# Optimization experiments

Hardware: AMD Instinct MI355X
Metric: run time of the kernel (lower is better)

The kernel has to match this reference:

```python
import jax, jax.numpy as jnp
import numpy as np

BN, SN = 16, 64
C, T, FY, FX = 480, 8, 28, 28
OS = 8            # roialign output_size
NDF = 256
K = 64            # n_clusters
ALPHA = 1.0
IMG_W, IMG_H = 1920.0, 1080.0
SPATIAL_SCALE = 1.0


def _roi_align(feat, boxes):
    """torchvision RoIAlign with sampling_ratio=1, aligned=True.
    feat: [bn, C, H, W]; boxes: [bn, sn, 4] (x1,y1,x2,y2) in feature coords.
    Returns [bn, sn, C, OS, OS]."""
    bn, c, H, W = feat.shape
    xy1 = boxes[..., 0:2] * SPATIAL_SCALE - 0.5   # aligned=True offset
    xy2 = boxes[..., 2:4] * SPATIAL_SCALE - 0.5
    bin_wh = (xy2 - xy1) / OS                     # [bn,sn,2]
    ctr = jnp.arange(OS, dtype=feat.dtype) + 0.5  # one sample per bin (ratio=1)
    xs = xy1[..., 0:1] + ctr * bin_wh[..., 0:1]   # [bn,sn,OS]
    ys = xy1[..., 1:2] + ctr * bin_wh[..., 1:2]
    X = xs[:, :, None, :]                         # [bn,sn,1,OS]
    Y = ys[:, :, :, None]                         # [bn,sn,OS,1]
    valid = (Y > -1.0) & (Y < H) & (X > -1.0) & (X < W)
    x = jnp.clip(X, 0.0, W - 1.0)
    y = jnp.clip(Y, 0.0, H - 1.0)
    x0 = jnp.floor(x).astype(jnp.int32)
    y0 = jnp.floor(y).astype(jnp.int32)
    x1 = jnp.minimum(x0 + 1, W - 1)
    y1 = jnp.minimum(y0 + 1, H - 1)
    lx = x - x0
    ly = y - y0
    fhw = jnp.transpose(feat, (0, 2, 3, 1))       # [bn,H,W,C]
    g = jax.vmap(lambda f, yy, xx: f[yy, xx])     # broadcasting gather -> [bn,sn,OS,OS,C]
    v00 = g(fhw, y0, x0); v01 = g(fhw, y0, x1)
    v10 = g(fhw, y1, x0); v11 = g(fhw, y1, x1)
    wy0, wy1 = (1.0 - ly)[..., None], ly[..., None]
    wx0, wx1 = (1.0 - lx)[..., None], lx[..., None]
    out = v00 * wy0 * wx0 + v01 * wy0 * wx1 + v10 * wy1 * wx0 + v11 * wy1 * wx1
    out = jnp.where(valid[..., None], out, 0.0)
    return jnp.transpose(out, (0, 1, 4, 2, 3))    # [bn,sn,C,OS,OS] (torch layout)


def setup_inputs() -> dict:
    key = jax.random.key(0)
    ks = jax.random.split(key, 6)
    z_vis = jax.random.normal(ks[0], (BN, C, T, FY, FX), jnp.float32)
    # valid boxes (x1<x2, y1<y2), fully inside the image -> no NaN padding rows
    tl = jax.random.uniform(ks[1], (BN, SN, 2)) * jnp.array([IMG_W * 0.5, IMG_H * 0.5])
    wh = jax.random.uniform(ks[2], (BN, SN, 2)) * jnp.array([IMG_W * 0.4, IMG_H * 0.4]) + 16.0
    bboxs = jnp.concatenate([tl, tl + wh], axis=-1).astype(jnp.float32)
    W_vis = jax.random.normal(ks[3], (C * OS * OS, NDF), jnp.float32) / np.sqrt(C * OS * OS)
    b_vis = jnp.zeros((NDF,), jnp.float32)
    W_spc = jax.random.normal(ks[4], (1, NDF), jnp.float32)
    b_spc = jnp.zeros((NDF,), jnp.float32)
    centroids = jax.random.normal(ks[5], (K, NDF), jnp.float32) * 0.1
    return {"z_vis": z_vis, "bboxs": bboxs, "W_vis": W_vis, "b_vis": b_vis,
            "W_spc": W_spc, "b_spc": b_spc, "centroids": centroids}


def reference(z_vis, bboxs, W_vis, b_vis, W_spc, b_spc, centroids):
    bn, sn = bboxs.shape[:2]
    # scale image-coord boxes to feature-map coords
    scale = jnp.array([FX / IMG_W, FY / IMG_H], dtype=z_vis.dtype)
    boxes_f = (bboxs.reshape(bn, sn, 2, 2) * scale).reshape(bn, sn, 4)
    feat = z_vis[:, :, -1]                                   # last temporal frame [bn,C,fy,fx]
    roi = _roi_align(feat, boxes_f).reshape(bn, sn, -1)      # [bn,sn,C*OS*OS]
    z_v = roi @ W_vis + b_vis                                # visual embedding [bn,sn,NDF]
    # spatial embedding: normalized distance of bbox center to image center (detached)
    b2 = bboxs.reshape(bn, sn, 2, 2)
    ctr = b2[:, :, 0] + (b2[:, :, 1] - b2[:, :, 0]) * 0.5    # [bn,sn,2]
    img_c = jnp.array([IMG_W / 2.0, IMG_H / 2.0], dtype=z_vis.dtype)
    norms = jnp.linalg.norm(ctr - img_c, axis=-1, keepdims=True) / jnp.linalg.norm(img_c)
    norms = jax.lax.stop_gradient(norms)                     # .detach() in original
    z_s = norms @ W_spc + b_spc                              # [bn,sn,NDF]
    z = z_v + z_s
    # Student-t soft assignment on L2 distance (NOT squared, as in the source)
    d = jnp.linalg.norm(z[:, :, None, :] - centroids, axis=-1)   # [bn,sn,K]
    s_un = (1.0 + d / ALPHA) ** (-(ALPHA + 1.0) / 2.0)
    s = s_un / jnp.sum(s_un, axis=-1, keepdims=True)
    c = jnp.argmax(s, axis=-1)
    return z, s, c
```

## Files before the change

### kernel.cpp

```cpp
#include <hip/hip_runtime.h>
#include <cstdint>
#include <cstddef>

#define BN_   16
#define C_    480
#define T_    8
#define FY_   28
#define FX_   28
#define NDF_  256
#define KC_   64
#define M_    1024
#define KD_   30720
#define PLANE_ 784
#define CHSTRIDE_ (T_*PLANE_)
#define CT_   (C_*CHSTRIDE_)
#define KS_   32
#define KCH_  960
#define BK_   32
#define NSTEP_ (KCH_/BK_)
#define MT_   32
#define APAD_ 40

typedef __attribute__((ext_vector_type(8))) short bf16x8;
typedef __attribute__((ext_vector_type(4))) float f32x4;

__device__ __forceinline__ unsigned rne_bf16(float f) {
    union { float f; unsigned u; } v; v.f = f;
    return v.u + 0x7FFFu + ((v.u >> 16) & 1u);
}
__device__ __forceinline__ float bfbits_to_f(unsigned r) {
    union { unsigned u; float f; } v; v.u = r & 0xFFFF0000u;
    return v.f;
}

__global__ __launch_bounds__(256)
void convert_w(const float* __restrict__ W, unsigned short* __restrict__ Wt_hi,
               unsigned short* __restrict__ Wt_lo) {
    __shared__ unsigned short th[64][68];
    __shared__ unsigned short tl[64][68];
    const int k0 = blockIdx.x * 64, n0 = blockIdx.y * 64;
    const int t = threadIdx.x;
    const int sub = t >> 4, off4 = (t & 15) * 4;
    #pragma unroll
    for (int p = 0; p < 4; ++p) {
        const int kr = p * 16 + sub;
        const float4 v = *(const float4*)&W[(size_t)(k0 + kr) * NDF_ + n0 + off4];
        const float vv[4] = { v.x, v.y, v.z, v.w };
        #pragma unroll
        for (int e = 0; e < 4; ++e) {
            const unsigned rh = rne_bf16(vv[e]);
            const unsigned rl = rne_bf16(vv[e] - bfbits_to_f(rh));
            th[kr][off4 + e] = (unsigned short)(rh >> 16);
            tl[kr][off4 + e] = (unsigned short)(rl >> 16);
        }
    }
    __syncthreads();
    #pragma unroll
    for (int p = 0; p < 4; ++p) {
        const int nr = p * 16 + sub;
        ushort4 oh, ol;
        oh.x = th[off4 + 0][nr]; oh.y = th[off4 + 1][nr];
        oh.z = th[off4 + 2][nr]; oh.w = th[off4 + 3][nr];
        ol.x = tl[off4 + 0][nr]; ol.y = tl[off4 + 1][nr];
        ol.z = tl[off4 + 2][nr]; ol.w = tl[off4 + 3][nr];
        *(ushort4*)&Wt_hi[(size_t)(n0 + nr) * KD_ + k0 + off4] = oh;
        *(ushort4*)&Wt_lo[(size_t)(n0 + nr) * KD_ + k0 + off4] = ol;
    }
}

__global__ void convert_cent(const float* __restrict__ cent, float* __restrict__ centT) {
    const int k = blockIdx.x;
    const int j = threadIdx.x;
    centT[(size_t)j * KC_ + k] = cent[(size_t)k * NDF_ + j];
}

__global__ __launch_bounds__(256, 4)
void gemm_fused(const float* __restrict__ z_vis, const unsigned short* __restrict__ Wt_hi,
                const unsigned short* __restrict__ Wt_lo, const float* __restrict__ bboxs,
                float* __restrict__ part) {
    __shared__ short Ah[MT_ * APAD_];
    __shared__ short Al[MT_ * APAD_];
    __shared__ unsigned short Bh[256 * 32];
    __shared__ unsigned short Bl[256 * 32];
    const int t = threadIdx.x;
    const int ks = blockIdx.x, mi = blockIdx.y;
    const int lane = t & 63, wid = t >> 6;
    const int kbase = ks * KCH_;

    const int m = t >> 3, q = t & 7;
    const int roi = mi * MT_ + m;
    const int bn = mi >> 1;

    int xi0[4], xi1[4];
    float xw0[4], xw1[4];
    int ye0, ye1, yo0, yo1;
    float ywe0, ywe1, ywo0, ywo1;
    {
        const float bx1 = bboxs[roi * 4 + 0], by1 = bboxs[roi * 4 + 1];
        const float bx2 = bboxs[roi * 4 + 2], by2 = bboxs[roi * 4 + 3];
        const float sx = 28.0f / 1920.0f, sy = 28.0f / 1080.0f;
        const float lo_x = bx1 * sx - 0.5f;
        const float binw_x = (bx2 * sx - 0.5f - lo_x) * 0.125f;
        const float lo_y = by1 * sy - 0.5f;
        const float binw_y = (by2 * sy - 0.5f - lo_y) * 0.125f;
        #pragma unroll
        for (int j = 0; j < 4; ++j) {
            const int b = (q & 1) * 4 + j;
            const float pos = lo_x + ((float)b + 0.5f) * binw_x;
            const float vx = (pos > -1.0f && pos < 28.0f) ? 1.0f : 0.0f;
            const float pc = fminf(fmaxf(pos, 0.0f), 27.0f);
            const float p0 = floorf(pc);
            const float lx = pc - p0;
            xi0[j] = (int)p0;
            xi1[j] = min(xi0[j] + 1, 27);
            xw0[j] = vx * (1.0f - lx);
            xw1[j] = vx * lx;
        }
        #pragma unroll
        for (int par = 0; par < 2; ++par) {
            const int by = par * 4 + (q >> 1);
            const float pos = lo_y + ((float)by + 0.5f) * binw_y;
            const float vy = (pos > -1.0f && pos < 28.0f) ? 1.0f : 0.0f;
            const float pc = fminf(fmaxf(pos, 0.0f), 27.0f);
            const float p0 = floorf(pc);
            const float ly = pc - p0;
            const int y0 = (int)p0, y1 = min(y0 + 1, 27);
            const float w0 = vy * (1.0f - ly), w1 = vy * ly;
            if (par == 0) { ye0 = y0; ye1 = y1; ywe0 = w0; ywe1 = w1; }
            else          { yo0 = y0; yo1 = y1; ywo0 = w0; ywo1 = w1; }
        }
    }
    const float* plane = z_vis + (size_t)bn * CT_ + (size_t)(T_ - 1) * PLANE_;

    const int brow_l = lane >> 2;
    const int bkoff = (lane & 3) * 8;

    auto stage_B = [&](int s) {
        #pragma unroll
        for (int qq = 0; qq < 4; ++qq) {
            const int rbase = qq * 64 + wid * 16;
            const size_t goff = (size_t)(rbase + brow_l) * KD_ + kbase + s * BK_ + bkoff;
            __builtin_amdgcn_global_load_lds(
                (const __attribute__((address_space(1))) void*)(Wt_hi + goff),
                (__attribute__((address_space(3))) void*)&Bh[rbase * 32], 16, 0, 0);
            __builtin_amdgcn_global_load_lds(
                (const __attribute__((address_space(1))) void*)(Wt_lo + goff),
                (__attribute__((address_space(3))) void*)&Bl[rbase * 32], 16, 0, 0);
        }
    };
    auto stage_A = [&](int s) {
        const int cch = ks * 15 + (s >> 1);
        const float* pl = plane + (size_t)cch * CHSTRIDE_;
        const int sodd = s & 1;
        const int y0 = sodd ? yo0 : ye0, y1 = sodd ? yo1 : ye1;
        const float wy0 = sodd ? ywo0 : ywe0, wy1 = sodd ? ywo1 : ywe1;
        const float* r0p = pl + y0 * FX_;
        const float* r1p = pl + y1 * FX_;
        unsigned rh[4], rl[4];
        #pragma unroll
        for (int j = 0; j < 4; ++j) {
            const float v00 = r0p[xi0[j]], v01 = r0p[xi1[j]];
            const float v10 = r1p[xi0[j]], v11 = r1p[xi1[j]];
            const float val = wy0 * (xw0[j] * v00 + xw1[j] * v01)
                            + wy1 * (xw0[j] * v10 + xw1[j] * v11);
            rh[j] = rne_bf16(val);
            rl[j] = rne_bf16(val - bfbits_to_f(rh[j]));
        }
        const unsigned ph0 = __builtin_amdgcn_perm(rh[1], rh[0], 0x07060302u);
        const unsigned ph1 = __builtin_amdgcn_perm(rh[3], rh[2], 0x07060302u);
        const unsigned pl0 = __builtin_amdgcn_perm(rl[1], rl[0], 0x07060302u);
        const unsigned pl1 = __builtin_amdgcn_perm(rl[3], rl[2], 0x07060302u);
        *(uint2*)&Ah[m * APAD_ + q * 4] = make_uint2(ph0, ph1);
        *(uint2*)&Al[m * APAD_ + q * 4] = make_uint2(pl0, pl1);
    };

    f32x4 acc[2][4] = {};
    const int fr = lane & 15, fq = lane >> 4;

    stage_B(0);
    stage_A(0);

    for (int s = 0; s < NSTEP_; ++s) {
        __syncthreads();

        bf16x8 afh[2], afl[2], bh[4], bl[4];
        #pragma unroll
        for (int i = 0; i < 2; ++i) {
            afh[i] = *(const bf16x8*)&Ah[(i * 16 + fr) * APAD_ + fq * 8];
            afl[i] = *(const bf16x8*)&Al[(i * 16 + fr) * APAD_ + fq * 8];
        }
        #pragma unroll
        for (int j = 0; j < 4; ++j) {
            bh[j] = *(const bf16x8*)&Bh[(wid * 64 + j * 16 + fr) * 32 + fq * 8];
            bl[j] = *(const bf16x8*)&Bl[(wid * 64 + j * 16 + fr) * 32 + fq * 8];
        }
        __syncthreads();

        if (s + 1 < NSTEP_) {
            stage_B(s + 1);
            stage_A(s + 1);
        }

        #pragma unroll
        for (int j = 0; j < 4; ++j)
            #pragma unroll
            for (int i = 0; i < 2; ++i) {
                acc[i][j] = __builtin_amdgcn_mfma_f32_16x16x32_bf16(afh[i], bh[j], acc[i][j], 0, 0, 0);
                acc[i][j] = __builtin_amdgcn_mfma_f32_16x16x32_bf16(afl[i], bh[j], acc[i][j], 0, 0, 0);
                acc[i][j] = __builtin_amdgcn_mfma_f32_16x16x32_bf16(afh[i], bl[j], acc[i][j], 0, 0, 0);
            }
    }

    float* pb = part + (size_t)ks * M_ * NDF_;
    #pragma unroll
    for (int i = 0; i < 2; ++i) {
        const int row = mi * MT_ + i * 16 + fq * 4;
        #pragma unroll
        for (int j = 0; j < 4; ++j) {
            const int col = wid * 64 + j * 16 + fr;
            #pragma unroll
            for (int r = 0; r < 4; ++r)
                pb[(size_t)(row + r) * NDF_ + col] = acc[i][j][r];
        }
    }
}

__global__ __launch_bounds__(256)
void cluster_kernel(const float* __restrict__ part, const float* __restrict__ bboxs,
                    const float* __restrict__ b_vis, const float* __restrict__ W_spc,
                    const float* __restrict__ b_spc, const float* __restrict__ centT,
                    float* __restrict__ out) {
    const int row = blockIdx.x, t = threadIdx.x;
    __shared__ float zs[NDF_];
    __shared__ float dp[4][KC_];

    float a = 0.0f;
    #pragma unroll
    for (int kp = 0; kp < KS_; ++kp)
        a += part[(size_t)kp * M_ * NDF_ + (size_t)row * NDF_ + t];

    const float x1 = bboxs[row * 4 + 0], y1 = bboxs[row * 4 + 1];
    const float x2 = bboxs[row * 4 + 2], y2 = bboxs[row * 4 + 3];
    const float cx = x1 + (x2 - x1) * 0.5f - 960.0f;
    const float cy = y1 + (y2 - y1) * 0.5f - 540.0f;
    const float nrm = sqrtf(cx * cx + cy * cy) / sqrtf(960.0f * 960.0f + 540.0f * 540.0f);

    const float zj = a + b_vis[t] + nrm * W_spc[t] + b_spc[t];
    zs[t] = zj;
    out[(size_t)row * NDF_ + t] = zj;
    __syncthreads();

    const int k = t & 63, qq = t >> 6;
    {
        float d2 = 0.0f;
        const float* ct = centT + (size_t)qq * 64 * KC_;
        #pragma unroll 8
        for (int j = 0; j < 64; ++j) {
            const float df = zs[qq * 64 + j] - ct[(size_t)j * KC_ + k];
            d2 += df * df;
        }
        dp[qq][k] = d2;
    }
    __syncthreads();

    if (t < 64) {
        const float d = sqrtf(dp[0][t] + dp[1][t] + dp[2][t] + dp[3][t]);
        const float su = 1.0f / (1.0f + d);
        float sum = su;
        #pragma unroll
        for (int mk = 1; mk < 64; mk <<= 1) sum += __shfl_xor(sum, mk, 64);
        out[(size_t)M_ * NDF_ + (size_t)row * KC_ + t] = su / sum;
        float v = d; int idx = t;
        #pragma unroll
        for (int mk = 1; mk < 64; mk <<= 1) {
            const float ov = __shfl_xor(v, mk, 64);
            const int oi = __shfl_xor(idx, mk, 64);
            if (ov < v || (ov == v && oi < idx)) { v = ov; idx = oi; }
        }
        if (t == 0)
            out[(size_t)M_ * NDF_ + (size_t)M_ * KC_ + row] = (float)idx;
    }
}

extern "C" void kernel_launch(void* const* d_in, const int* in_sizes, int n_in,
                              void* d_out, int out_size, void* d_ws, size_t ws_size,
                              hipStream_t stream) {
    const float* z_vis = (const float*)d_in[0];
    const float* bboxs = (const float*)d_in[1];
    const float* W_vis = (const float*)d_in[2];
    const float* b_vis = (const float*)d_in[3];
    const float* W_spc = (const float*)d_in[4];
    const float* b_spc = (const float*)d_in[5];
    const float* cent  = (const float*)d_in[6];
    float* out = (float*)d_out;

    char* ws = (char*)d_ws;
    unsigned short* Wt_hi = (unsigned short*)ws;
    unsigned short* Wt_lo = (unsigned short*)(ws + 15728640);
    float*          centT = (float*)(ws + 2 * 15728640);
    float*          part  = (float*)(ws + 2 * 15728640 + 65536);

    convert_w<<<dim3(KD_ / 64, NDF_ / 64), 256, 0, stream>>>(W_vis, Wt_hi, Wt_lo);
    convert_cent<<<KC_, 256, 0, stream>>>(cent, centT);
    gemm_fused<<<dim3(KS_, M_ / MT_), 256, 0, stream>>>(z_vis, Wt_hi, Wt_lo, bboxs, part);
    cluster_kernel<<<M_, 256, 0, stream>>>(part, bboxs, b_vis, W_spc, b_spc, centT, out);
}
```

Measured before the change: 413.3 us.

## Stage feature-map channel plane in LDS and build A tiles per channel

Each 28x28 channel plane of the last frame is now copied into shared memory by one wave using async global-to-LDS loads, instead of every thread gathering bilinear samples straight from global memory. Each thread now produces all 8 x-bins for one y-bin, and a whole channel (64 K values) of the A tile is built at once with a wider padded row. The main loop is split into two half-steps per channel, with the next plane's load overlapped with compute. This targets the scattered global gathers in the ROI-align stage, at the cost of more LDS and registers per block, so the occupancy hint drops from 4 to 3 blocks.

Result: no change. 408.3 us (-1.2%).

```diff
diff --git a/kernel.cpp b/kernel.cpp
--- a/kernel.cpp
+++ b/kernel.cpp
@@ -16,10 +16,9 @@
 #define CT_   (C_*CHSTRIDE_)
 #define KS_   32
 #define KCH_  960
-#define BK_   32
-#define NSTEP_ (KCH_/BK_)
+#define NCH_  15
 #define MT_   32
-#define APAD_ 40
+#define APAD_ 72
 
 typedef __attribute__((ext_vector_type(8))) short bf16x8;
 typedef __attribute__((ext_vector_type(4))) float f32x4;
@@ -74,7 +73,7 @@
     centT[(size_t)j * KC_ + k] = cent[(size_t)k * NDF_ + j];
 }
 
-__global__ __launch_bounds__(256, 4)
+__global__ __launch_bounds__(256, 3)
 void gemm_fused(const float* __restrict__ z_vis, const unsigned short* __restrict__ Wt_hi,
                 const unsigned short* __restrict__ Wt_lo, const float* __restrict__ bboxs,
                 float* __restrict__ part) {
@@ -82,19 +81,21 @@
     __shared__ short Al[MT_ * APAD_];
     __shared__ unsigned short Bh[256 * 32];
     __shared__ unsigned short Bl[256 * 32];
+    __shared__ float Pl[PLANE_];
+
     const int t = threadIdx.x;
     const int ks = blockIdx.x, mi = blockIdx.y;
     const int lane = t & 63, wid = t >> 6;
     const int kbase = ks * KCH_;
 
-    const int m = t >> 3, q = t & 7;
+    const int m = t >> 3, by = t & 7;
     const int roi = mi * MT_ + m;
     const int bn = mi >> 1;
 
-    int xi0[4], xi1[4];
-    float xw0[4], xw1[4];
-    int ye0, ye1, yo0, yo1;
-    float ywe0, ywe1, ywo0, ywo1;
+    int xi0[8], xi1[8];
+    float xw0[8], xw1[8];
+    int yr0, yr1;
+    float wy0v, wy1v;
     {
         const float bx1 = bboxs[roi * 4 + 0], by1 = bboxs[roi * 4 + 1];
         const float bx2 = bboxs[roi * 4 + 2], by2 = bboxs[roi * 4 + 3];
@@ -104,42 +105,50 @@
         const float lo_y = by1 * sy - 0.5f;
         const float binw_y = (by2 * sy - 0.5f - lo_y) * 0.125f;
         #pragma unroll
-        for (int j = 0; j < 4; ++j) {
-            const int b = (q & 1) * 4 + j;
+        for (int b = 0; b < 8; ++b) {
             const float pos = lo_x + ((float)b + 0.5f) * binw_x;
             const float vx = (pos > -1.0f && pos < 28.0f) ? 1.0f : 0.0f;
             const float pc = fminf(fmaxf(pos, 0.0f), 27.0f);
             const float p0 = floorf(pc);
             const float lx = pc - p0;
-            xi0[j] = (int)p0;
-            xi1[j] = min(xi0[j] + 1, 27);
-            xw0[j] = vx * (1.0f - lx);
-            xw1[j] = vx * lx;
-        }
-        #pragma unroll
-        for (int par = 0; par < 2; ++par) {
-            const int by = par * 4 + (q >> 1);
-            const float pos = lo_y + ((float)by + 0.5f) * binw_y;
-            const float vy = (pos > -1.0f && pos < 28.0f) ? 1.0f : 0.0f;
-            const float pc = fminf(fmaxf(pos, 0.0f), 27.0f);
-            const float p0 = floorf(pc);
-            const float ly = pc - p0;
-            const int y0 = (int)p0, y1 = min(y0 + 1, 27);
-            const float w0 = vy * (1.0f - ly), w1 = vy * ly;
-            if (par == 0) { ye0 = y0; ye1 = y1; ywe0 = w0; ywe1 = w1; }
-            else          { yo0 = y0; yo1 = y1; ywo0 = w0; ywo1 = w1; }
-        }
+            xi0[b] = (int)p0;
+            xi1[b] = min(xi0[b] + 1, 27);
+            xw0[b] = vx * (1.0f - lx);
+            xw1[b] = vx * lx;
+        }
+        const float pos = lo_y + ((float)by + 0.5f) * binw_y;
+        const float vy = (pos > -1.0f && pos < 28.0f) ? 1.0f : 0.0f;
+        const float pc = fminf(fmaxf(pos, 0.0f), 27.0f);
+        const float p0 = floorf(pc);
+        const float ly = pc - p0;
+        const int y0 = (int)p0, y1 = min(y0 + 1, 27);
+        yr0 = y0 * FX_; yr1 = y1 * FX_;
+        wy0v = vy * (1.0f - ly); wy1v = vy * ly;
     }
     const float* plane = z_vis + (size_t)bn * CT_ + (size_t)(T_ - 1) * PLANE_;
 
     const int brow_l = lane >> 2;
     const int bkoff = (lane & 3) * 8;
 
+    auto plane_load = [&](int cc) {
+        if (wid != 0) return;
+        const char* gb = (const char*)(plane + (size_t)(ks * NCH_ + cc) * CHSTRIDE_);
+        #pragma unroll
+        for (int i = 0; i < 3; ++i)
+            __builtin_amdgcn_global_load_lds(
+                (const __attribute__((address_space(1))) void*)(gb + (i * 64 + lane) * 16),
+                (__attribute__((address_space(3))) void*)((char*)Pl + i * 1024), 16, 0, 0);
+        if (lane < 4)
+            __builtin_amdgcn_global_load_lds(
+                (const __attribute__((address_space(1))) void*)(gb + (192 + lane) * 16),
+                (__attribute__((address_space(3))) void*)((char*)Pl + 3072), 16, 0, 0);
+    };
+
     auto stage_B = [&](int s) {
         #pragma unroll
         for (int qq = 0; qq < 4; ++qq) {
             const int rbase = qq * 64 + wid * 16;
-            const size_t goff = (size_t)(rbase + brow_l) * KD_ + kbase + s * BK_ + bkoff;
+            const size_t goff = (size_t)(rbase + brow_l) * KD_ + kbase + s * 32 + bkoff;
             __builtin_amdgcn_global_load_lds(
                 (const __attribute__((address_space(1))) void*)(Wt_hi + goff),
                 (__attribute__((address_space(3))) void*)&Bh[rbase * 32], 16, 0, 0);
@@ -148,67 +157,74 @@
                 (__attribute__((address_space(3))) void*)&Bl[rbase * 32], 16, 0, 0);
         }
     };
-    auto stage_A = [&](int s) {
-        const int cch = ks * 15 + (s >> 1);
-        const float* pl = plane + (size_t)cch * CHSTRIDE_;
-        const int sodd = s & 1;
-        const int y0 = sodd ? yo0 : ye0, y1 = sodd ? yo1 : ye1;
-        const float wy0 = sodd ? ywo0 : ywe0, wy1 = sodd ? ywo1 : ywe1;
-        const float* r0p = pl + y0 * FX_;
-        const float* r1p = pl + y1 * FX_;
-        unsigned rh[4], rl[4];
-        #pragma unroll
-        for (int j = 0; j < 4; ++j) {
-            const float v00 = r0p[xi0[j]], v01 = r0p[xi1[j]];
-            const float v10 = r1p[xi0[j]], v11 = r1p[xi1[j]];
-            const float val = wy0 * (xw0[j] * v00 + xw1[j] * v01)
-                            + wy1 * (xw0[j] * v10 + xw1[j] * v11);
-            rh[j] = rne_bf16(val);
-            rl[j] = rne_bf16(val - bfbits_to_f(rh[j]));
-        }
-        const unsigned ph0 = __builtin_amdgcn_perm(rh[1], rh[0], 0x07060302u);
-        const unsigned ph1 = __builtin_amdgcn_perm(rh[3], rh[2], 0x07060302u);
-        const unsigned pl0 = __builtin_amdgcn_perm(rl[1], rl[0], 0x07060302u);
-        const unsigned pl1 = __builtin_amdgcn_perm(rl[3], rl[2], 0x07060302u);
-        *(uint2*)&Ah[m * APAD_ + q * 4] = make_uint2(ph0, ph1);
-        *(uint2*)&Al[m * APAD_ + q * 4] = make_uint2(pl0, pl1);
+
+    auto stage_A = [&]() {
+        unsigned rh[8], rl[8];
+        #pragma unroll
+        for (int b = 0; b < 8; ++b) {
+            const float v00 = Pl[yr0 + xi0[b]], v01 = Pl[yr0 + xi1[b]];
+            const float v10 = Pl[yr1 + xi0[b]], v11 = Pl[yr1 + xi1[b]];
+            const float val = wy0v * (xw0[b] * v00 + xw1[b] * v01)
+                            + wy1v * (xw0[b] * v10 + xw1[b] * v11);
+            rh[b] = rne_bf16(val);
+            rl[b] = rne_bf16(val - bfbits_to_f(rh[b]));
+        }
+        const uint4 hh = make_uint4(__builtin_amdgcn_perm(rh[1], rh[0], 0x07060302u),
+                                    __builtin_amdgcn_perm(rh[3], rh[2], 0x07060302u),
+                                    __builtin_amdgcn_perm(rh[5], rh[4], 0x07060302u),
+                                    __builtin_amdgcn_perm(rh[7], rh[6], 0x07060302u));
+        const uint4 ll = make_uint4(__builtin_amdgcn_perm(rl[1], rl[0], 0x07060302u),
+                                    __builtin_amdgcn_perm(rl[3], rl[2], 0x07060302u),
+                                    __builtin_amdgcn_perm(rl[5], rl[4], 0x07060302u),
+                                    __builtin_amdgcn_perm(rl[7], rl[6], 0x07060302u));
+        *(uint4*)&Ah[m * APAD_ + by * 8] = hh;
+        *(uint4*)&Al[m * APAD_ + by * 8] = ll;
     };
 
+    const int fr = lane & 15, fq = lane >> 4;
     f32x4 acc[2][4] = {};
-    const int fr = lane & 15, fq = lane >> 4;
-
+
+    plane_load(0);
     stage_B(0);
-    stage_A(0);
-
-    for (int s = 0; s < NSTEP_; ++s) {
-        __syncthreads();
-
-        bf16x8 afh[2], afl[2], bh[4], bl[4];
-        #pragma unroll
-        for (int i = 0; i < 2; ++i) {
-            afh[i] = *(const bf16x8*)&Ah[(i * 16 + fr) * APAD_ + fq * 8];
-            afl[i] = *(const bf16x8*)&Al[(i * 16 + fr) * APAD_ + fq * 8];
-        }
-        #pragma unroll
-        for (int j = 0; j < 4; ++j) {
-            bh[j] = *(const bf16x8*)&Bh[(wid * 64 + j * 16 + fr) * 32 + fq * 8];
-            bl[j] = *(const bf16x8*)&Bl[(wid * 64 + j * 16 + fr) * 32 + fq * 8];
-        }
-        __syncthreads();
-
-        if (s + 1 < NSTEP_) {
-            stage_B(s + 1);
-            stage_A(s + 1);
-        }
-
-        #pragma unroll
-        for (int j = 0; j < 4; ++j)
+    __syncthreads();
+    stage_A();
+
+    for (int cc = 0; cc < NCH_; ++cc) {
+        #pragma unroll
+        for (int half = 0; half < 2; ++half) {
+            const int s = 2 * cc + half;
+            __syncthreads();
+
+            bf16x8 afh[2], afl[2], bh[4], bl[4];
             #pragma unroll
             for (int i = 0; i < 2; ++i) {
-                acc[i][j] = __builtin_amdgcn_mfma_f32_16x16x32_bf16(afh[i], bh[j], acc[i][j], 0, 0, 0);
-                acc[i][j] = __builtin_amdgcn_mfma_f32_16x16x32_bf16(afl[i], bh[j], acc[i][j], 0, 0, 0);
-                acc[i][j] = __builtin_amdgcn_mfma_f32_16x16x32_bf16(afh[i], bl[j], acc[i][j], 0, 0, 0);
+                afh[i] = *(const bf16x8*)&Ah[(i * 16 + fr) * APAD_ + half * 32 + fq * 8];
+                afl[i] = *(const bf16x8*)&Al[(i * 16 + fr) * APAD_ + half * 32 + fq * 8];
             }
+            #pragma unroll
+            for (int j = 0; j < 4; ++j) {
+                bh[j] = *(const bf16x8*)&Bh[(wid * 64 + j * 16 + fr) * 32 + fq * 8];
+                bl[j] = *(const bf16x8*)&Bl[(wid * 64 + j * 16 + fr) * 32 + fq * 8];
+            }
+            __syncthreads();
+
+            if (half == 0) {
+                stage_B(s + 1);
+                if (cc + 1 < NCH_) plane_load(cc + 1);
+            } else if (cc + 1 < NCH_) {
+                stage_B(s + 1);
+                stage_A();
+            }
+
+            #pragma unroll
+            for (int j = 0; j < 4; ++j)
+                #pragma unroll
+                for (int i = 0; i < 2; ++i) {
+                    acc[i][j] = __builtin_amdgcn_mfma_f32_16x16x32_bf16(afh[i], bh[j], acc[i][j], 0, 0, 0);
+                    acc[i][j] = __builtin_amdgcn_mfma_f32_16x16x32_bf16(afl[i], bh[j], acc[i][j], 0, 0, 0);
+                    acc[i][j] = __builtin_amdgcn_mfma_f32_16x16x32_bf16(afh[i], bl[j], acc[i][j], 0, 0, 0);
+                }
+        }
     }
 
     float* pb = part + (size_t)ks * M_ * NDF_;
```
